# Optimization experiments

Hardware: AMD Instinct MI355X
Metric: run time of the kernel (lower is better)

The kernel has to match this reference:

```python
import jax, jax.numpy as jnp
import numpy as np

R_MIN = 0.01
R_MAX = 0.6
H = 32            # polar radial bins (after pooling)
W = 64            # polar angular bins (after pooling)
UP_R = 10         # radial upsampling factor
UP_T = 10         # angular upsampling factor
ATT_ALPHA = 5.0
B, C, IMG = 64, 3, 224


def _conv(x, w, b):
    # NCHW valid conv, stride 1 (matches nn.Conv2d default padding=0)
    y = jax.lax.conv_general_dilated(x, w, (1, 1), 'VALID',
                                     dimension_numbers=('NCHW', 'OIHW', 'NCHW'))
    return y + b[None, :, None, None]


def _maxpool2(x):
    return jax.lax.reduce_window(x, -jnp.inf, jax.lax.max,
                                 (1, 1, 2, 2), (1, 1, 2, 2), 'VALID')


def _grid_sample_border(x, grid):
    # F.grid_sample, bilinear, padding_mode='border', align_corners=False
    Bn, Cn, Hi, Wi = x.shape
    ix = ((grid[..., 0] + 1.0) * Wi - 1.0) * 0.5   # x-coord -> width index
    iy = ((grid[..., 1] + 1.0) * Hi - 1.0) * 0.5   # y-coord -> height index
    x0f = jnp.floor(ix)
    y0f = jnp.floor(iy)
    wx = (ix - x0f)[..., None]
    wy = (iy - y0f)[..., None]
    x0 = jnp.clip(x0f.astype(jnp.int32), 0, Wi - 1)
    x1 = jnp.clip(x0f.astype(jnp.int32) + 1, 0, Wi - 1)
    y0 = jnp.clip(y0f.astype(jnp.int32), 0, Hi - 1)
    y1 = jnp.clip(y0f.astype(jnp.int32) + 1, 0, Hi - 1)
    bidx = jnp.arange(Bn)[:, None, None]
    v00 = x[bidx, :, y0, x0]   # [B,Hg,Wg,C]
    v01 = x[bidx, :, y0, x1]
    v10 = x[bidx, :, y1, x0]
    v11 = x[bidx, :, y1, x1]
    out = (v00 * (1 - wx) * (1 - wy) + v01 * wx * (1 - wy)
           + v10 * (1 - wx) * wy + v11 * wx * wy)
    return jnp.transpose(out, (0, 3, 1, 2))  # [B,C,Hg,Wg]


def setup_inputs() -> dict:
    key = jax.random.key(0)
    ks = jax.random.split(key, 10)
    x = jax.random.normal(ks[0], (B, C, IMG, IMG), dtype=jnp.float32)
    l_t_prev = jax.random.uniform(ks[1], (B, 2), dtype=jnp.float32)
    conv1_w = jax.random.normal(ks[2], (6, C, 5, 5), dtype=jnp.float32) * 0.1
    conv1_b = jnp.zeros((6,), jnp.float32)
    conv2_w = jax.random.normal(ks[3], (16, 6, 5, 5), dtype=jnp.float32) * 0.1
    conv2_b = jnp.zeros((16,), jnp.float32)
    fc1_w = jax.random.normal(ks[4], (8, 16), dtype=jnp.float32) * 0.1
    fc1_b = jnp.zeros((8,), jnp.float32)
    fc2_w = jax.random.normal(ks[5], (2, 8), dtype=jnp.float32) * 0.1
    fc2_b = jnp.zeros((2,), jnp.float32)
    return dict(x=x, l_t_prev=l_t_prev, conv1_w=conv1_w, conv1_b=conv1_b,
                conv2_w=conv2_w, conv2_b=conv2_b, fc1_w=fc1_w, fc1_b=fc1_b,
                fc2_w=fc2_w, fc2_b=fc2_b)


def reference(x, l_t_prev, conv1_w, conv1_b, conv2_w, conv2_b,
              fc1_w, fc1_b, fc2_w, fc2_b):
    # --- attention branch: conv -> maxpool -> conv -> GAP -> fc -> sigmoid ---
    h = _conv(x, conv1_w, conv1_b)
    h = _maxpool2(h)
    h = _conv(h, conv2_w, conv2_b)
    feat = h.mean(axis=(2, 3))                     # AdaptiveAvgPool2d(1), [B,16]
    h = jax.nn.relu(feat @ fc1_w.T + fc1_b)
    weight = jax.nn.sigmoid(h @ fc2_w.T + fc2_b) * ATT_ALPHA   # [B,2]
    # --- per-batch log-polar grid ---
    Hg, Wg = H * UP_R, W * UP_T
    angle = 2.0 * jnp.pi * jnp.arange(Wg, dtype=jnp.float32) / Wg
    unit = jnp.stack([jnp.sin(angle), jnp.cos(angle)], axis=-1)   # [Wg,2]
    start = jnp.log(R_MIN * weight[:, 0])
    stop = jnp.log(R_MAX * weight[:, 1])
    t = jnp.arange(Hg, dtype=jnp.float32) / (Hg - 1)
    radii = jnp.exp(start[:, None] + (stop - start)[:, None] * t[None])  # [B,Hg]
    grid = radii[:, :, None, None] * unit[None, None]     # [B,Hg,Wg,2]
    grid = grid + l_t_prev[:, None, None, :]
    # --- irregular bilinear sampling + box filter ---
    sampled = _grid_sample_border(x, grid)                 # [B,C,Hg,Wg]
    Bn, Cn = sampled.shape[:2]
    pooled = sampled.reshape(Bn, Cn, H, UP_R, W, UP_T).mean(axis=(3, 5))
    return pooled, weight
```

## Files before the change

### kernel.cpp

```cpp
#include <hip/hip_runtime.h>
#include <math.h>

#define Bn    64
#define Cn    3
#define IMG   224
#define PLANE (IMG*IMG)
#define C1    6
#define P1    110
#define P2    106
#define NVALID (P2*P2)
#define Hh    32
#define Ww    64
#define UPR   10
#define UPT   10
#define Hg    (Hh*UPR)
#define Wg    (Ww*UPT)
#define POOLED_SIZE (Bn*Cn*Hh*Ww)
#define RPB   4
#define NCHUNK ((P1 + RPB - 1) / RPB)
#define PSTRIDE 152

typedef unsigned short u16;
typedef float v2f __attribute__((ext_vector_type(2)));

#define PART_FLOATS ((size_t)Bn * NCHUNK * PSTRIDE)
#define X4B_U16     ((size_t)Bn * PLANE * 4)
#define WS_NEEDED   ((PART_FLOATS + Bn * 2) * 4 + X4B_U16 * 2)

__device__ __forceinline__ u16 f2bf(float f) {
    union { unsigned int u; float f; } c; c.f = f;
    unsigned int r = c.u + 0x7fffu + ((c.u >> 16) & 1u);
    return (u16)(r >> 16);
}
__device__ __forceinline__ float bf2f(u16 v) {
    union { unsigned int u; float f; } c; c.u = ((unsigned int)v) << 16;
    return c.f;
}

__device__ __forceinline__ void load_pairs(v2f* P, const float* rp) {
    const float4 a = *(const float4*)rp;
    const float4 c = *(const float4*)(rp + 4);
    P[0] = (v2f){a.x, a.y};
    P[1] = (v2f){a.y, a.z};
    P[2] = (v2f){a.z, a.w};
    P[3] = (v2f){a.w, c.x};
    P[4] = (v2f){c.x, c.y};
    P[5] = (v2f){c.y, c.z};
    P[6] = (v2f){c.z, c.w};
}

__global__ __launch_bounds__(256) void k1_fused(
    const float* __restrict__ x,
    const float* __restrict__ w1,
    const float* __restrict__ b1,
    float* __restrict__ partial,
    u16* __restrict__ x4b,
    int do_pack)
{
    __shared__ __attribute__((aligned(16))) float xs[3][12][224];
    __shared__ float psum[RPB][PSTRIDE];

    const int b    = blockIdx.y;
    const int tid  = threadIdx.x;
    const int wid  = tid >> 6;
    const int lane = tid & 63;

    const float* xb = x + (size_t)b * (Cn * PLANE);

    for (int half = 0; half < 2; ++half) {
        const int chunk = 2 * blockIdx.x + half;
        const int y0 = chunk * RPB;
        const int gybase = 2 * y0;

        for (int i = tid; i < 3 * 12 * 56; i += 256) {
            const int ic  = i / (12 * 56);
            const int rem = i - ic * (12 * 56);
            const int r   = rem / 56;
            const int c4  = rem - r * 56;
            const int gy  = gybase + r;
            if (gy < IMG)
                *(float4*)(&xs[ic][r][c4 * 4]) =
                    *(const float4*)(xb + ic * PLANE + gy * IMG + c4 * 4);
        }
        __syncthreads();

        if (do_pack) {
            u16* ob = x4b + (size_t)b * PLANE * 4;
            for (int i = tid; i < 8 * IMG; i += 256) {
                const int r   = i / IMG;
                const int col = i - r * IMG;
                const int gy  = gybase + r;
                ushort4 v;
                v.x = f2bf(xs[0][r][col]);
                v.y = f2bf(xs[1][r][col]);
                v.z = f2bf(xs[2][r][col]);
                v.w = 0;
                *(ushort4*)(ob + ((size_t)gy * IMG + col) * 4) = v;
            }
        }

        const int y = y0 + wid;
        const bool rowvalid = (y < P1);
        const bool active = (lane < 55) && rowvalid;

        float pp0[C1], pp1[C1];
        if (active) {
            v2f accT01[C1], accT23[C1], accB01[C1], accB23[C1];
            #pragma unroll
            for (int oc = 0; oc < C1; ++oc) {
                const float bv = b1[oc];
                const v2f bvv = (v2f){bv, bv};
                accT01[oc] = bvv; accT23[oc] = bvv;
                accB01[oc] = bvv; accB23[oc] = bvv;
            }

            #pragma unroll
            for (int ic = 0; ic < 3; ++ic) {
                v2f Pa[7], Pb[7];
                load_pairs(Pa, &xs[ic][2 * wid][4 * lane]);
                load_pairs(Pb, &xs[ic][2 * wid + 1][4 * lane]);
                #pragma unroll
                for (int ky = 0; ky < 5; ++ky) {
                    const v2f* Pt = (ky & 1) ? Pb : Pa;
                    const v2f* Po = (ky & 1) ? Pa : Pb;
                    #pragma unroll
                    for (int oc = 0; oc < C1; ++oc) {
                        const float* wrow = w1 + ((oc * 3 + ic) * 25 + ky * 5);
                        #pragma unroll
                        for (int kx = 0; kx < 5; ++kx) {
                            const float wv = wrow[kx];
                            const v2f wvv = (v2f){wv, wv};
                            accT01[oc] += Pt[kx]     * wvv;
                            accT23[oc] += Pt[kx + 2] * wvv;
                            accB01[oc] += Po[kx]     * wvv;
                            accB23[oc] += Po[kx + 2] * wvv;
                        }
                    }
                    if (ky < 4)
                        load_pairs((ky & 1) ? Pb : Pa,
                                   &xs[ic][2 * wid + ky + 2][4 * lane]);
                }
            }

            #pragma unroll
            for (int oc = 0; oc < C1; ++oc) {
                pp0[oc] = fmaxf(fmaxf(accT01[oc].x, accT01[oc].y),
                                fmaxf(accB01[oc].x, accB01[oc].y));
                pp1[oc] = fmaxf(fmaxf(accT23[oc].x, accT23[oc].y),
                                fmaxf(accB23[oc].x, accB23[oc].y));
            }
        } else {
            #pragma unroll
            for (int oc = 0; oc < C1; ++oc) { pp0[oc] = 0.0f; pp1[oc] = 0.0f; }
        }

        #pragma unroll
        for (int oc = 0; oc < C1; ++oc) {
            float s = pp0[oc] + pp1[oc];
            #pragma unroll
            for (int off = 32; off > 0; off >>= 1) s += __shfl_xor(s, off, 64);
            const float c0   = __shfl(pp0[oc], 0, 64);
            const float c1   = __shfl(pp1[oc], 0, 64);
            const float c2   = __shfl(pp0[oc], 1, 64);
            const float c3   = __shfl(pp1[oc], 1, 64);
            const float c106 = __shfl(pp0[oc], 53, 64);
            const float c107 = __shfl(pp1[oc], 53, 64);
            const float c108 = __shfl(pp0[oc], 54, 64);
            const float c109 = __shfl(pp1[oc], 54, 64);
            const float w0v = s - (c106 + c107 + c108 + c109);
            const float w1v = s - c0 - (c107 + c108 + c109);
            const float w2v = s - (c0 + c1) - (c108 + c109);
            const float w3v = s - (c0 + c1 + c2) - c109;
            const float w4v = s - (c0 + c1 + c2 + c3);
            if (lane < 25) {
                const int ky = lane / 5;
                const int kx = lane % 5;
                float wv = w0v;
                wv = (kx == 1) ? w1v : wv;
                wv = (kx == 2) ? w2v : wv;
                wv = (kx == 3) ? w3v : wv;
                wv = (kx == 4) ? w4v : wv;
                const bool valid = rowvalid && ((unsigned)(y - ky) <= 105u);
                psum[wid][oc * 25 + lane] = valid ? wv : 0.0f;
            }
        }
        __syncthreads();

        if (tid < 150) {
            const float v = psum[0][tid] + psum[1][tid] + psum[2][tid] + psum[3][tid];
            partial[((size_t)b * NCHUNK + chunk) * PSTRIDE + tid] = v;
        }
    }
}

__global__ __launch_bounds__(256) void k2_head(
    const float* __restrict__ partial, const float* __restrict__ w2,
    const float* __restrict__ b2, const float* __restrict__ fc1w,
    const float* __restrict__ fc1b, const float* __restrict__ fc2w,
    const float* __restrict__ fc2b, float* __restrict__ wt_ws,
    float* __restrict__ out)
{
    const int b = blockIdx.x;
    const int tid = threadIdx.x;
    __shared__ float wsb[150];
    __shared__ float sfeat[16];
    __shared__ float sh[8];

    if (tid < 150) {
        const float* p = partial + (size_t)b * NCHUNK * PSTRIDE + tid;
        float s = 0.0f;
        #pragma unroll
        for (int c = 0; c < NCHUNK; ++c) s += p[c * PSTRIDE];
        wsb[tid] = s;
    }
    __syncthreads();
    if (tid < 16) {
        float s = 0.0f;
        for (int j = 0; j < 150; ++j) s += w2[tid * 150 + j] * wsb[j];
        sfeat[tid] = b2[tid] + s * (1.0f / (float)NVALID);
    }
    __syncthreads();
    if (tid < 8) {
        float s = fc1b[tid];
        #pragma unroll
        for (int j = 0; j < 16; ++j) s += fc1w[tid * 16 + j] * sfeat[j];
        sh[tid] = fmaxf(s, 0.0f);
    }
    __syncthreads();
    if (tid < 2) {
        float s = fc2b[tid];
        #pragma unroll
        for (int j = 0; j < 8; ++j) s += fc2w[tid * 8 + j] * sh[j];
        float sig = (s >= 0.0f) ? (1.0f / (1.0f + expf(-s)))
                                : (expf(s) / (1.0f + expf(s)));
        const float wgt = 5.0f * sig;
        wt_ws[b * 2 + tid] = wgt;
        out[POOLED_SIZE + b * 2 + tid] = wgt;
    }
}

__device__ __forceinline__ void sample_coords(
    float gxn, float gyn, int& x0, int& y0, float& wx, float& wy)
{
    float ix = ((gxn + 1.0f) * (float)IMG - 1.0f) * 0.5f;
    float iy = ((gyn + 1.0f) * (float)IMG - 1.0f) * 0.5f;
    ix = fminf(fmaxf(ix, 0.0f), (float)(IMG - 1));
    iy = fminf(fmaxf(iy, 0.0f), (float)(IMG - 1));
    x0 = (int)ix; if (x0 > IMG - 2) x0 = IMG - 2;
    y0 = (int)iy; if (y0 > IMG - 2) y0 = IMG - 2;
    wx = ix - (float)x0;
    wy = iy - (float)y0;
}

__global__ __launch_bounds__(640) void k3_sample_pool_bf16(
    const u16* __restrict__ x4b,
    const float* __restrict__ ltp,
    const float* __restrict__ wt,
    float* __restrict__ out)
{
    __shared__ float part[3 * Wg];

    const int L = blockIdx.x;
    const int q = L >> 3;
    const int h = q & 31;
    const int b = (L & 7) + 8 * (q >> 5);
    const int tid = threadIdx.x;

    const float w0 = wt[b * 2 + 0];
    const float w1 = wt[b * 2 + 1];
    const float l0 = ltp[b * 2 + 0];
    const float l1 = ltp[b * 2 + 1];
    const float start = logf(0.01f * w0);
    const float stop  = logf(0.6f  * w1);
    const float dr = stop - start;

    const float angle = 6.283185307179586f * (float)tid / (float)Wg;
    const float sn = sinf(angle);
    const float cs = cosf(angle);

    const u16* xb4 = x4b + (size_t)b * PLANE * 4;

    const float ratio = expf(dr * (1.0f / (float)(Hg - 1)));
    float r = expf(start + dr * ((float)(h * UPR) / (float)(Hg - 1)));

    float acc0 = 0.0f, acc1 = 0.0f, acc2 = 0.0f;
    #pragma unroll
    for (int i = 0; i < UPR; ++i) {
        int x0, y0; float wx, wy;
        sample_coords(r * sn + l0, r * cs + l1, x0, y0, wx, wy);
        r *= ratio;

        const u16* base = xb4 + ((size_t)(y0 * IMG + x0)) * 4;
        const ushort4 a00 = *(const ushort4*)(base);
        const ushort4 a01 = *(const ushort4*)(base + 4);
        const ushort4 a10 = *(const ushort4*)(base + IMG * 4);
        const ushort4 a11 = *(const ushort4*)(base + IMG * 4 + 4);

        const float wx0 = 1.0f - wx, wy0 = 1.0f - wy;
        const float w00 = wx0 * wy0, w01 = wx * wy0;
        const float w10 = wx0 * wy,  w11 = wx * wy;

        acc0 += w00*bf2f(a00.x) + w01*bf2f(a01.x) + w10*bf2f(a10.x) + w11*bf2f(a11.x);
        acc1 += w00*bf2f(a00.y) + w01*bf2f(a01.y) + w10*bf2f(a10.y) + w11*bf2f(a11.y);
        acc2 += w00*bf2f(a00.z) + w01*bf2f(a01.z) + w10*bf2f(a10.z) + w11*bf2f(a11.z);
    }
    part[0 * Wg + tid] = acc0;
    part[1 * Wg + tid] = acc1;
    part[2 * Wg + tid] = acc2;
    __syncthreads();

    if (tid < Cn * Ww) {
        const int c = tid / Ww;
        const int w = tid % Ww;
        const float* p = part + c * Wg + w * UPT;
        float s = 0.0f;
        #pragma unroll
        for (int j = 0; j < UPT; ++j) s += p[j];
        out[(((size_t)b * Cn + c) * Hh + h) * Ww + w] = s * (1.0f / (UPR * UPT));
    }
}

__global__ __launch_bounds__(640) void k3_sample_pool_nchw(
    const float* __restrict__ x, const float* __restrict__ ltp,
    const float* __restrict__ wt, float* __restrict__ out)
{
    __shared__ float part[3 * Wg];
    const int L = blockIdx.x;
    const int q = L >> 3;
    const int h = q & 31;
    const int b = (L & 7) + 8 * (q >> 5);
    const int tid = threadIdx.x;

    const float w0 = wt[b * 2 + 0];
    const float w1 = wt[b * 2 + 1];
    const float l0 = ltp[b * 2 + 0];
    const float l1 = ltp[b * 2 + 1];
    const float start = logf(0.01f * w0);
    const float stop  = logf(0.6f  * w1);
    const float dr = stop - start;
    const float angle = 6.283185307179586f * (float)tid / (float)Wg;
    const float sn = sinf(angle);
    const float cs = cosf(angle);
    const float* xb = x + (size_t)b * Cn * PLANE;

    const float ratio = expf(dr * (1.0f / (float)(Hg - 1)));
    float r = expf(start + dr * ((float)(h * UPR) / (float)(Hg - 1)));

    float acc0 = 0.0f, acc1 = 0.0f, acc2 = 0.0f;
    #pragma unroll
    for (int i = 0; i < UPR; ++i) {
        int x0, y0; float wx, wy;
        sample_coords(r * sn + l0, r * cs + l1, x0, y0, wx, wy);
        r *= ratio;
        const float wx0 = 1.0f - wx, wy0 = 1.0f - wy;
        const float w00 = wx0 * wy0, w01 = wx * wy0;
        const float w10 = wx0 * wy,  w11 = wx * wy;
        const int o00 = y0 * IMG + x0;
        acc0 += w00*xb[o00] + w01*xb[o00+1] + w10*xb[o00+IMG] + w11*xb[o00+IMG+1];
        const float* x1p = xb + PLANE;
        acc1 += w00*x1p[o00] + w01*x1p[o00+1] + w10*x1p[o00+IMG] + w11*x1p[o00+IMG+1];
        const float* x2p = xb + 2 * PLANE;
        acc2 += w00*x2p[o00] + w01*x2p[o00+1] + w10*x2p[o00+IMG] + w11*x2p[o00+IMG+1];
    }
    part[0 * Wg + tid] = acc0;
    part[1 * Wg + tid] = acc1;
    part[2 * Wg + tid] = acc2;
    __syncthreads();

    if (tid < Cn * Ww) {
        const int c = tid / Ww;
        const int w = tid % Ww;
        const float* p = part + c * Wg + w * UPT;
        float s = 0.0f;
        #pragma unroll
        for (int j = 0; j < UPT; ++j) s += p[j];
        out[(((size_t)b * Cn + c) * Hh + h) * Ww + w] = s * (1.0f / (UPR * UPT));
    }
}

extern "C" void kernel_launch(void* const* d_in, const int* in_sizes, int n_in,
                              void* d_out, int out_size, void* d_ws, size_t ws_size,
                              hipStream_t stream) {
    const float* x       = (const float*)d_in[0];
    const float* ltp     = (const float*)d_in[1];
    const float* conv1_w = (const float*)d_in[2];
    const float* conv1_b = (const float*)d_in[3];
    const float* conv2_w = (const float*)d_in[4];
    const float* conv2_b = (const float*)d_in[5];
    const float* fc1_w   = (const float*)d_in[6];
    const float* fc1_b   = (const float*)d_in[7];
    const float* fc2_w   = (const float*)d_in[8];
    const float* fc2_b   = (const float*)d_in[9];
    float* out = (float*)d_out;

    const int do_pack = (ws_size >= WS_NEEDED) ? 1 : 0;

    float* part_ws = (float*)d_ws;
    float* wt_ws   = part_ws + PART_FLOATS;
    u16*   x4b     = (u16*)(wt_ws + Bn * 2);

    k1_fused<<<dim3(NCHUNK / 2, Bn), dim3(256), 0, stream>>>(
        x, conv1_w, conv1_b, part_ws, x4b, do_pack);
    k2_head<<<dim3(Bn), dim3(256), 0, stream>>>(part_ws, conv2_w, conv2_b,
                                                fc1_w, fc1_b, fc2_w, fc2_b,
                                                wt_ws, out);
    if (do_pack)
        k3_sample_pool_bf16<<<dim3(Hh * Bn), dim3(Wg), 0, stream>>>(x4b, ltp, wt_ws, out);
    else
        k3_sample_pool_nchw<<<dim3(Hh * Bn), dim3(Wg), 0, stream>>>(x, ltp, wt_ws, out);
}
```

Before: 176.3 us.

## Fuse attention head into sampling kernel and drop k2 launch

The tiny k2_head kernel is removed on the packed path. Each sampling block now reduces the conv partial sums itself and evaluates conv2, GAP and the FC/sigmoid head before sampling. k1 now writes per-row partials directly, without the shared-memory reduction and the extra barrier, and loads 20 input rows in a single pass instead of two halves. The sin, cos, log and exp calls become fast intrinsics. In exchange, the head work is recomputed redundantly in all 32 h-blocks per batch, and the partial buffer grows fourfold.

```diff
diff --git a/kernel.cpp b/kernel.cpp
--- a/kernel.cpp
+++ b/kernel.cpp
@@ -17,23 +17,25 @@
 #define Wg    (Ww*UPT)
 #define POOLED_SIZE (Bn*Cn*Hh*Ww)
 #define RPB   4
-#define NCHUNK ((P1 + RPB - 1) / RPB)
+#define NCHUNK 28
+#define PCHUNK (NCHUNK * RPB)
 #define PSTRIDE 152
 
 typedef unsigned short u16;
+typedef unsigned int   u32;
 typedef float v2f __attribute__((ext_vector_type(2)));
 
-#define PART_FLOATS ((size_t)Bn * NCHUNK * PSTRIDE)
+#define PART_FLOATS ((size_t)Bn * PCHUNK * PSTRIDE)
 #define X4B_U16     ((size_t)Bn * PLANE * 4)
 #define WS_NEEDED   ((PART_FLOATS + Bn * 2) * 4 + X4B_U16 * 2)
 
 __device__ __forceinline__ u16 f2bf(float f) {
-    union { unsigned int u; float f; } c; c.f = f;
-    unsigned int r = c.u + 0x7fffu + ((c.u >> 16) & 1u);
+    union { u32 u; float f; } c; c.f = f;
+    u32 r = c.u + 0x7fffu + ((c.u >> 16) & 1u);
     return (u16)(r >> 16);
 }
 __device__ __forceinline__ float bf2f(u16 v) {
-    union { unsigned int u; float f; } c; c.u = ((unsigned int)v) << 16;
+    union { u32 u; float f; } c; c.u = ((u32)v) << 16;
     return c.f;
 }
 
@@ -57,49 +59,48 @@
     u16* __restrict__ x4b,
     int do_pack)
 {
-    __shared__ __attribute__((aligned(16))) float xs[3][12][224];
-    __shared__ float psum[RPB][PSTRIDE];
+    __shared__ __attribute__((aligned(16))) float xs[3][20][224];
 
     const int b    = blockIdx.y;
+    const int q    = blockIdx.x;
     const int tid  = threadIdx.x;
     const int wid  = tid >> 6;
     const int lane = tid & 63;
 
     const float* xb = x + (size_t)b * (Cn * PLANE);
-
-    for (int half = 0; half < 2; ++half) {
-        const int chunk = 2 * blockIdx.x + half;
-        const int y0 = chunk * RPB;
-        const int gybase = 2 * y0;
-
-        for (int i = tid; i < 3 * 12 * 56; i += 256) {
-            const int ic  = i / (12 * 56);
-            const int rem = i - ic * (12 * 56);
-            const int r   = rem / 56;
-            const int c4  = rem - r * 56;
+    const int gybase = 16 * q;
+
+    for (int i = tid; i < 3 * 20 * 56; i += 256) {
+        const int ic  = i / (20 * 56);
+        const int rem = i - ic * (20 * 56);
+        const int r   = rem / 56;
+        const int c4  = rem - r * 56;
+        const int gy  = gybase + r;
+        if (gy < IMG)
+            *(float4*)(&xs[ic][r][c4 * 4]) =
+                *(const float4*)(xb + ic * PLANE + gy * IMG + c4 * 4);
+    }
+    __syncthreads();
+
+    if (do_pack) {
+        u16* ob = x4b + (size_t)b * PLANE * 4;
+        for (int i = tid; i < 16 * IMG; i += 256) {
+            const int r   = i / IMG;
+            const int col = i - r * IMG;
             const int gy  = gybase + r;
-            if (gy < IMG)
-                *(float4*)(&xs[ic][r][c4 * 4]) =
-                    *(const float4*)(xb + ic * PLANE + gy * IMG + c4 * 4);
+            ushort4 v;
+            v.x = f2bf(xs[0][r][col]);
+            v.y = f2bf(xs[1][r][col]);
+            v.z = f2bf(xs[2][r][col]);
+            v.w = 0;
+            *(ushort4*)(ob + ((size_t)gy * IMG + col) * 4) = v;
         }
-        __syncthreads();
-
-        if (do_pack) {
-            u16* ob = x4b + (size_t)b * PLANE * 4;
-            for (int i = tid; i < 8 * IMG; i += 256) {
-                const int r   = i / IMG;
-                const int col = i - r * IMG;
-                const int gy  = gybase + r;
-                ushort4 v;
-                v.x = f2bf(xs[0][r][col]);
-                v.y = f2bf(xs[1][r][col]);
-                v.z = f2bf(xs[2][r][col]);
-                v.w = 0;
-                *(ushort4*)(ob + ((size_t)gy * IMG + col) * 4) = v;
-            }
-        }
-
-        const int y = y0 + wid;
+    }
+
+    #pragma unroll
+    for (int c = 0; c < 2; ++c) {
+        const int y = 8 * q + 4 * c + wid;
+        const int rowbase = 2 * wid + 8 * c;
         const bool rowvalid = (y < P1);
         const bool active = (lane < 55) && rowvalid;
 
@@ -117,8 +118,8 @@
             #pragma unroll
             for (int ic = 0; ic < 3; ++ic) {
                 v2f Pa[7], Pb[7];
-                load_pairs(Pa, &xs[ic][2 * wid][4 * lane]);
-                load_pairs(Pb, &xs[ic][2 * wid + 1][4 * lane]);
+                load_pairs(Pa, &xs[ic][rowbase][4 * lane]);
+                load_pairs(Pb, &xs[ic][rowbase + 1][4 * lane]);
                 #pragma unroll
                 for (int ky = 0; ky < 5; ++ky) {
                     const v2f* Pt = (ky & 1) ? Pb : Pa;
@@ -138,7 +139,7 @@
                     }
                     if (ky < 4)
                         load_pairs((ky & 1) ? Pb : Pa,
-                                   &xs[ic][2 * wid + ky + 2][4 * lane]);
+                                   &xs[ic][rowbase + ky + 2][4 * lane]);
                 }
             }
 
@@ -154,6 +155,8 @@
             for (int oc = 0; oc < C1; ++oc) { pp0[oc] = 0.0f; pp1[oc] = 0.0f; }
         }
 
+        float* dst = partial +
+            ((size_t)b * PCHUNK + (2 * q + c) * RPB + wid) * PSTRIDE;
         #pragma unroll
         for (int oc = 0; oc < C1; ++oc) {
             float s = pp0[oc] + pp1[oc];
@@ -181,15 +184,133 @@
                 wv = (kx == 3) ? w3v : wv;
                 wv = (kx == 4) ? w4v : wv;
                 const bool valid = rowvalid && ((unsigned)(y - ky) <= 105u);
-                psum[wid][oc * 25 + lane] = valid ? wv : 0.0f;
+                dst[oc * 25 + lane] = valid ? wv : 0.0f;
             }
         }
-        __syncthreads();
-
-        if (tid < 150) {
-            const float v = psum[0][tid] + psum[1][tid] + psum[2][tid] + psum[3][tid];
-            partial[((size_t)b * NCHUNK + chunk) * PSTRIDE + tid] = v;
+    }
+}
+
+__device__ __forceinline__ void sample_coords(
+    float gxn, float gyn, int& x0, int& y0, float& wx, float& wy)
+{
+    float ix = ((gxn + 1.0f) * (float)IMG - 1.0f) * 0.5f;
+    float iy = ((gyn + 1.0f) * (float)IMG - 1.0f) * 0.5f;
+    ix = fminf(fmaxf(ix, 0.0f), (float)(IMG - 1));
+    iy = fminf(fmaxf(iy, 0.0f), (float)(IMG - 1));
+    x0 = (int)ix; if (x0 > IMG - 2) x0 = IMG - 2;
+    y0 = (int)iy; if (y0 > IMG - 2) y0 = IMG - 2;
+    wx = ix - (float)x0;
+    wy = iy - (float)y0;
+}
+
+__global__ __launch_bounds__(640) void k3_fused(
+    const u16* __restrict__ x4b,
+    const float* __restrict__ ltp,
+    const float* __restrict__ partial,
+    const float* __restrict__ w2, const float* __restrict__ b2,
+    const float* __restrict__ fc1w, const float* __restrict__ fc1b,
+    const float* __restrict__ fc2w, const float* __restrict__ fc2b,
+    float* __restrict__ out)
+{
+    __shared__ float part[3 * Wg];
+    __shared__ float red[4][150];
+    __shared__ float wsb[150];
+    __shared__ float wt2[2];
+
+    const int L = blockIdx.x;
+    const int qq = L >> 3;
+    const int h = qq & 31;
+    const int b = (L & 7) + 8 * (qq >> 5);
+    const int tid = threadIdx.x;
+
+    const float angle = 6.283185307179586f * (float)tid / (float)Wg;
+    const float sn = __sinf(angle);
+    const float cs = __cosf(angle);
+
+    if (tid < 600) {
+        const int g = tid / 150;
+        const int e = tid - g * 150;
+        const float* p = partial + ((size_t)b * PCHUNK + g * 28) * PSTRIDE + e;
+        float s = 0.0f;
+        #pragma unroll 7
+        for (int c = 0; c < 28; ++c) s += p[c * PSTRIDE];
+        red[g][e] = s;
+    }
+    __syncthreads();
+    if (tid < 150)
+        wsb[tid] = red[0][tid] + red[1][tid] + red[2][tid] + red[3][tid];
+    __syncthreads();
+    if (tid < 64) {
+        const int fi = tid & 15;
+        float s = 0.0f;
+        for (int j = 0; j < 150; ++j) s += w2[fi * 150 + j] * wsb[j];
+        const float feat = b2[fi] + s * (1.0f / (float)NVALID);
+        const int hi = tid & 7;
+        float s1 = fc1b[hi];
+        #pragma unroll
+        for (int j = 0; j < 16; ++j) s1 += fc1w[hi * 16 + j] * __shfl(feat, j, 64);
+        const float hv = fmaxf(s1, 0.0f);
+        const int oi = tid & 1;
+        float s2 = fc2b[oi];
+        #pragma unroll
+        for (int j = 0; j < 8; ++j) s2 += fc2w[oi * 8 + j] * __shfl(hv, j, 64);
+        const float sig = (s2 >= 0.0f) ? (1.0f / (1.0f + __expf(-s2)))
+                                       : (__expf(s2) / (1.0f + __expf(s2)));
+        const float wgt = 5.0f * sig;
+        if (tid < 2) {
+            wt2[tid] = wgt;
+            if (h == 0) out[POOLED_SIZE + b * 2 + tid] = wgt;
         }
+    }
+    __syncthreads();
+
+    const float w0 = wt2[0];
+    const float w1 = wt2[1];
+    const float l0 = ltp[b * 2 + 0];
+    const float l1 = ltp[b * 2 + 1];
+    const float start = __logf(0.01f * w0);
+    const float stop  = __logf(0.6f  * w1);
+    const float dr = stop - start;
+
+    const u16* xb4 = x4b + (size_t)b * PLANE * 4;
+
+    const float ratio = __expf(dr * (1.0f / (float)(Hg - 1)));
+    float r = __expf(start + dr * ((float)(h * UPR) / (float)(Hg - 1)));
+
+    float acc0 = 0.0f, acc1 = 0.0f, acc2 = 0.0f;
+    #pragma unroll
+    for (int i = 0; i < UPR; ++i) {
+        int x0, y0; float wx, wy;
+        sample_coords(r * sn + l0, r * cs + l1, x0, y0, wx, wy);
+        r *= ratio;
+
+        const u16* base = xb4 + ((size_t)(y0 * IMG + x0)) * 4;
+        const ushort4 a00 = *(const ushort4*)(base);
+        const ushort4 a01 = *(const ushort4*)(base + 4);
+        const ushort4 a10 = *(const ushort4*)(base + IMG * 4);
+        const ushort4 a11 = *(const ushort4*)(base + IMG * 4 + 4);
+
+        const float wx0 = 1.0f - wx, wy0 = 1.0f - wy;
+        const float w00 = wx0 * wy0, w01 = wx * wy0;
+        const float w10 = wx0 * wy,  w11 = wx * wy;
+
+        acc0 += w00*bf2f(a00.x) + w01*bf2f(a01.x) + w10*bf2f(a10.x) + w11*bf2f(a11.x);
+        acc1 += w00*bf2f(a00.y) + w01*bf2f(a01.y) + w10*bf2f(a10.y) + w11*bf2f(a11.y);
+        acc2 += w00*bf2f(a00.z) + w01*bf2f(a01.z) + w10*bf2f(a10.z) + w11*bf2f(a11.z);
+    }
+    part[0 * Wg + tid] = acc0;
+    part[1 * Wg + tid] = acc1;
+    part[2 * Wg + tid] = acc2;
+    __syncthreads();
+
+    if (tid < Cn * Ww) {
+        const int c = tid / Ww;
+        const int w = tid % Ww;
+        const float* p = part + c * Wg + w * UPT;
+        float s = 0.0f;
+        #pragma unroll
+        for (int j = 0; j < UPT; ++j) s += p[j];
+        out[(((size_t)b * Cn + c) * Hh + h) * Ww + w] = s * (1.0f / (UPR * UPT));
     }
 }
 
@@ -207,10 +328,10 @@
     __shared__ float sh[8];
 
     if (tid < 150) {
-        const float* p = partial + (size_t)b * NCHUNK * PSTRIDE + tid;
-        float s = 0.0f;
-        #pragma unroll
-        for (int c = 0; c < NCHUNK; ++c) s += p[c * PSTRIDE];
+        const float* p = partial + (size_t)b * PCHUNK * PSTRIDE + tid;
+        float s = 0.0f;
+        #pragma unroll 8
+        for (int c = 0; c < PCHUNK; ++c) s += p[c * PSTRIDE];
         wsb[tid] = s;
     }
     __syncthreads();
@@ -239,96 +360,15 @@
     }
 }
 
-__device__ __forceinline__ void sample_coords(
-    float gxn, float gyn, int& x0, int& y0, float& wx, float& wy)
-{
-    float ix = ((gxn + 1.0f) * (float)IMG - 1.0f) * 0.5f;
-    float iy = ((gyn + 1.0f) * (float)IMG - 1.0f) * 0.5f;
-    ix = fminf(fmaxf(ix, 0.0f), (float)(IMG - 1));
-    iy = fminf(fmaxf(iy, 0.0f), (float)(IMG - 1));
-    x0 = (int)ix; if (x0 > IMG - 2) x0 = IMG - 2;
-    y0 = (int)iy; if (y0 > IMG - 2) y0 = IMG - 2;
-    wx = ix - (float)x0;
-    wy = iy - (float)y0;
-}
-
-__global__ __launch_bounds__(640) void k3_sample_pool_bf16(
-    const u16* __restrict__ x4b,
-    const float* __restrict__ ltp,
-    const float* __restrict__ wt,
-    float* __restrict__ out)
-{
-    __shared__ float part[3 * Wg];
-
-    const int L = blockIdx.x;
-    const int q = L >> 3;
-    const int h = q & 31;
-    const int b = (L & 7) + 8 * (q >> 5);
-    const int tid = threadIdx.x;
-
-    const float w0 = wt[b * 2 + 0];
-    const float w1 = wt[b * 2 + 1];
-    const float l0 = ltp[b * 2 + 0];
-    const float l1 = ltp[b * 2 + 1];
-    const float start = logf(0.01f * w0);
-    const float stop  = logf(0.6f  * w1);
-    const float dr = stop - start;
-
-    const float angle = 6.283185307179586f * (float)tid / (float)Wg;
-    const float sn = sinf(angle);
-    const float cs = cosf(angle);
-
-    const u16* xb4 = x4b + (size_t)b * PLANE * 4;
-
-    const float ratio = expf(dr * (1.0f / (float)(Hg - 1)));
-    float r = expf(start + dr * ((float)(h * UPR) / (float)(Hg - 1)));
-
-    float acc0 = 0.0f, acc1 = 0.0f, acc2 = 0.0f;
-    #pragma unroll
-    for (int i = 0; i < UPR; ++i) {
-        int x0, y0; float wx, wy;
-        sample_coords(r * sn + l0, r * cs + l1, x0, y0, wx, wy);
-        r *= ratio;
-
-        const u16* base = xb4 + ((size_t)(y0 * IMG + x0)) * 4;
-        const ushort4 a00 = *(const ushort4*)(base);
-        const ushort4 a01 = *(const ushort4*)(base + 4);
-        const ushort4 a10 = *(const ushort4*)(base + IMG * 4);
-        const ushort4 a11 = *(const ushort4*)(base + IMG * 4 + 4);
-
-        const float wx0 = 1.0f - wx, wy0 = 1.0f - wy;
-        const float w00 = wx0 * wy0, w01 = wx * wy0;
-        const float w10 = wx0 * wy,  w11 = wx * wy;
-
-        acc0 += w00*bf2f(a00.x) + w01*bf2f(a01.x) + w10*bf2f(a10.x) + w11*bf2f(a11.x);
-        acc1 += w00*bf2f(a00.y) + w01*bf2f(a01.y) + w10*bf2f(a10.y) + w11*bf2f(a11.y);
-        acc2 += w00*bf2f(a00.z) + w01*bf2f(a01.z) + w10*bf2f(a10.z) + w11*bf2f(a11.z);
-    }
-    part[0 * Wg + tid] = acc0;
-    part[1 * Wg + tid] = acc1;
-    part[2 * Wg + tid] = acc2;
-    __syncthreads();
-
-    if (tid < Cn * Ww) {
-        const int c = tid / Ww;
-        const int w = tid % Ww;
-        const float* p = part + c * Wg + w * UPT;
-        float s = 0.0f;
-        #pragma unroll
-        for (int j = 0; j < UPT; ++j) s += p[j];
-        out[(((size_t)b * Cn + c) * Hh + h) * Ww + w] = s * (1.0f / (UPR * UPT));
-    }
-}
-
 __global__ __launch_bounds__(640) void k3_sample_pool_nchw(
     const float* __restrict__ x, const float* __restrict__ ltp,
     const float* __restrict__ wt, float* __restrict__ out)
 {
     __shared__ float part[3 * Wg];
     const int L = blockIdx.x;
-    const int q = L >> 3;
-    const int h = q & 31;
-    const int b = (L & 7) + 8 * (q >> 5);
+    const int qq = L >> 3;
+    const int h = qq & 31;
+    const int b = (L & 7) + 8 * (qq >> 5);
     const int tid = threadIdx.x;
 
     const float w0 = wt[b * 2 + 0];
@@ -399,13 +439,17 @@
     float* wt_ws   = part_ws + PART_FLOATS;
     u16*   x4b     = (u16*)(wt_ws + Bn * 2);
 
-    k1_fused<<<dim3(NCHUNK / 2, Bn), dim3(256), 0, stream>>>(
+    k1_fused<<<dim3(14, Bn), dim3(256), 0, stream>>>(
         x, conv1_w, conv1_b, part_ws, x4b, do_pack);
-    k2_head<<<dim3(Bn), dim3(256), 0, stream>>>(part_ws, conv2_w, conv2_b,
-                                                fc1_w, fc1_b, fc2_w, fc2_b,
-                                                wt_ws, out);
-    if (do_pack)
-        k3_sample_pool_bf16<<<dim3(Hh * Bn), dim3(Wg), 0, stream>>>(x4b, ltp, wt_ws, out);
-    else
+
+    if (do_pack) {
+        k3_fused<<<dim3(Hh * Bn), dim3(Wg), 0, stream>>>(
+            x4b, ltp, part_ws, conv2_w, conv2_b,
+            fc1_w, fc1_b, fc2_w, fc2_b, out);
+    } else {
+        k2_head<<<dim3(Bn), dim3(256), 0, stream>>>(part_ws, conv2_w, conv2_b,
+                                                    fc1_w, fc1_b, fc2_w, fc2_b,
+                                                    wt_ws, out);
         k3_sample_pool_nchw<<<dim3(Hh * Bn), dim3(Wg), 0, stream>>>(x, ltp, wt_ws, out);
-}
+    }
+}
```

Measured after the change: 191.8 us. +8.8%, slower.
